# Performance work log

Hardware: AMD Instinct MI355X
Metric: run time of the kernel (lower is better)

The kernel has to match this reference:

```python
import jax, jax.numpy as jnp
import numpy as np

E = 768      # embed_dim (hidden_size)
H = 12       # num_attention_heads
DH = E // H  # head_dim = 64
B, S = 8, 1024


def setup_inputs() -> dict:
    key = jax.random.key(0)
    ks = jax.random.split(key, 10)
    sc = 1.0 / np.sqrt(E)
    inp = {
        "hidden_state": jax.random.normal(ks[0], (B, S, E), dtype=jnp.float32),
        # per-head Q/K/V projections, stacked over heads: [H, E, DH]
        "Wq": jax.random.normal(ks[1], (H, E, DH), dtype=jnp.float32) * sc,
        "bq": jax.random.normal(ks[2], (H, DH), dtype=jnp.float32) * 0.02,
        "Wk": jax.random.normal(ks[3], (H, E, DH), dtype=jnp.float32) * sc,
        "bk": jax.random.normal(ks[4], (H, DH), dtype=jnp.float32) * 0.02,
        "Wv": jax.random.normal(ks[5], (H, E, DH), dtype=jnp.float32) * sc,
        "bv": jax.random.normal(ks[6], (H, DH), dtype=jnp.float32) * 0.02,
        # output projection: [E, E]
        "Wo": jax.random.normal(ks[7], (E, E), dtype=jnp.float32) * sc,
        "bo": jax.random.normal(ks[8], (E,), dtype=jnp.float32) * 0.02,
    }
    return inp


def reference(hidden_state, Wq, bq, Wk, bk, Wv, bv, Wo, bo):
    # Q/K/V per head: [B,S,E] x [H,E,D] -> [B,H,S,D]
    q = jnp.einsum("bse,hed->bhsd", hidden_state, Wq) + bq[None, :, None, :]
    k = jnp.einsum("bse,hed->bhsd", hidden_state, Wk) + bk[None, :, None, :]
    v = jnp.einsum("bse,hed->bhsd", hidden_state, Wv) + bv[None, :, None, :]
    scale = 1.0 / jnp.sqrt(jnp.asarray(DH, dtype=q.dtype))
    scores = jnp.einsum("bhsd,bhtd->bhst", q, k) * scale   # [B,H,S,S]
    weights = jax.nn.softmax(scores, axis=-1)
    attn = jnp.einsum("bhst,bhtd->bhsd", weights, v)        # [B,H,S,D]
    # concat heads (head order matches ModuleList concat): [B,S,H*D]=[B,S,E]
    x = attn.transpose(0, 2, 1, 3).reshape(hidden_state.shape[0], hidden_state.shape[1], E)
    return x @ Wo + bo
```

## Files before the change

### kernel.cpp

```cpp
#include <hip/hip_runtime.h>

typedef unsigned short u16;
typedef __bf16 bf16;
typedef bf16 bf16x8 __attribute__((ext_vector_type(8)));
typedef float f32x4 __attribute__((ext_vector_type(4)));
typedef u16 u16x4 __attribute__((ext_vector_type(4)));
typedef u16 u16x8 __attribute__((ext_vector_type(8)));

#define MROWS 8192
#define EDIM 768
#define NQKV 2304
#define NHEAD 12
#define DH 64
#define SEQ 1024
#define BATCH 8
#define BH 96
#define BHSD (BH * SEQ * DH)
#define KIT64 (EDIM / 64)

#if __has_builtin(__builtin_amdgcn_exp2f)
#define EXP2(x) __builtin_amdgcn_exp2f(x)
#else
#define EXP2(x) exp2f(x)
#endif

__device__ __forceinline__ u16 f2bf(float f) {
  bf16 b = (bf16)f;
  return __builtin_bit_cast(u16, b);
}

__device__ __forceinline__ void gload_lds16(const u16* g, u16* l) {
  __builtin_amdgcn_global_load_lds(
      (const __attribute__((address_space(1))) void*)g,
      (__attribute__((address_space(3))) void*)l, 16, 0, 0);
}


__global__ void cvt_x(const float* __restrict__ x, u16* __restrict__ xb, int n) {
  int i = (blockIdx.x * blockDim.x + threadIdx.x) * 4;
  if (i >= n) return;
  float4 v = *(const float4*)(x + i);
  u16x4 o;
  o[0] = f2bf(v.x); o[1] = f2bf(v.y); o[2] = f2bf(v.z); o[3] = f2bf(v.w);
  *(u16x4*)(xb + i) = o;
}

__global__ __launch_bounds__(256) void pack_w(
    const float* __restrict__ Wq, const float* __restrict__ Wk,
    const float* __restrict__ Wv, const float* __restrict__ Wo,
    u16* __restrict__ Wt, u16* __restrict__ Wot) {
  __shared__ float T[64][65];
  int bid = blockIdx.x;
  int tid = threadIdx.x;
  int c = tid & 63, r4 = tid >> 6;
  if (bid < 432) {
    int region = bid / 144, rem = bid - region * 144;
    int h = rem / 12, e0 = (rem - h * 12) * 64;
    const float* W = region == 0 ? Wq : (region == 1 ? Wk : Wv);
    for (int p = 0; p < 16; p++) {
      int er = r4 + p * 4;
      T[er][c] = W[(size_t)(h * EDIM + e0 + er) * DH + c];
    }
    __syncthreads();
    int nbase = region * EDIM + h * 64;
    for (int p = 0; p < 16; p++) {
      int dr = r4 + p * 4;
      Wt[(size_t)(nbase + dr) * EDIM + e0 + c] = f2bf(T[c][dr]);
    }
  } else {
    bid -= 432;
    int n0 = (bid / 12) * 64, e0 = (bid - (bid / 12) * 12) * 64;
    for (int p = 0; p < 16; p++) {
      int er = r4 + p * 4;
      T[er][c] = Wo[(size_t)(e0 + er) * EDIM + n0 + c];
    }
    __syncthreads();
    for (int p = 0; p < 16; p++) {
      int dr = r4 + p * 4;
      Wot[(size_t)(n0 + dr) * EDIM + e0 + c] = f2bf(T[c][dr]);
    }
  }
}

template <int BM, int BN, int NW>
__device__ __forceinline__ void gemm_core(
    const u16* __restrict__ A, const u16* __restrict__ Bt,
    u16* As, u16* Bs, int m0, int n0, int tid, f32x4 acc[4][4]) {
  constexpr int NT = NW * 64;
  constexpr int RPP = NT / 8;
  constexpr int AP = BM / RPP;
  constexpr int BP = BN / RPP;
  constexpr int WMN = BM / 64;
  int wv = __builtin_amdgcn_readfirstlane(tid >> 6);
  int lane = tid & 63, quad = lane >> 4, l16 = lane & 15;
  int wm = (wv % WMN) * 64, wn = (wv / WMN) * 64;
  int srow = tid >> 3, cpos = tid & 7;
  int swcol = (cpos ^ (srow & 7)) * 8;
  const u16* Ag = A + (size_t)(m0 + srow) * EDIM + swcol;
  const u16* Bg = Bt + (size_t)(n0 + srow) * EDIM + swcol;
  u16* Asl = As + srow * 64 + cpos * 8;
  u16* Bsl = Bs + srow * 64 + cpos * 8;

  for (int k = 0; k < KIT64; k++) {
    __syncthreads();
    const u16* ak = Ag + k * 64;
    const u16* bk = Bg + k * 64;
#pragma unroll
    for (int p = 0; p < AP; p++)
      gload_lds16(ak + (size_t)(p * RPP) * EDIM, Asl + p * RPP * 64);
#pragma unroll
    for (int p = 0; p < BP; p++)
      gload_lds16(bk + (size_t)(p * RPP) * EDIM, Bsl + p * RPP * 64);
    __syncthreads();
#pragma unroll
    for (int kh = 0; kh < 2; kh++) {
      bf16x8 af[4], bfr[4];
      for (int i = 0; i < 4; i++) {
        int row = wm + i * 16 + l16;
        af[i] = *(const bf16x8*)(As + row * 64 + (((kh * 4 + quad) ^ (row & 7))) * 8);
      }
      for (int j = 0; j < 4; j++) {
        int row = wn + j * 16 + l16;
        bfr[j] = *(const bf16x8*)(Bs + row * 64 + (((kh * 4 + quad) ^ (row & 7))) * 8);
      }
      for (int i = 0; i < 4; i++)
        for (int j = 0; j < 4; j++)
          acc[i][j] = __builtin_amdgcn_mfma_f32_16x16x32_bf16(af[i], bfr[j], acc[i][j], 0, 0, 0);
    }
  }
}

__global__ __launch_bounds__(256, 4) void gemm_qkv(
    const u16* __restrict__ A, const u16* __restrict__ Bt,
    const float* __restrict__ bq, const float* __restrict__ bk, const float* __restrict__ bv,
    u16* __restrict__ qkv) {
  __shared__ __align__(16) u16 As[128 * 64];
  __shared__ __align__(16) u16 Bs[128 * 64];
  int tid = threadIdx.x;
  int wv = tid >> 6, lane = tid & 63, quad = lane >> 4, l16 = lane & 15;
  int wm = (wv & 1) * 64, wn = (wv >> 1) * 64;
  int lin = blockIdx.y * 64 + blockIdx.x;
  int xcd = lin & 7, r8 = lin >> 3;
  int m0 = (xcd * 8 + (r8 & 7)) * 128;
  int n0 = (r8 >> 3) * 128;
  f32x4 acc[4][4] = {};
  gemm_core<128, 128, 4>(A, Bt, As, Bs, m0, n0, tid, acc);

  const float kQscale = 0.18033688011112042f;
  for (int i = 0; i < 4; i++) {
    int row0 = m0 + wm + i * 16 + quad * 4;
    for (int j = 0; j < 4; j++) {
      int n = n0 + wn + j * 16 + l16;
      int region = n / EDIM;
      int hd = n - region * EDIM;
      int h = hd >> 6, d = hd & 63;
      const float* bp = region == 0 ? bq : (region == 1 ? bk : bv);
      float bias = bp[hd];
      float scale = region == 0 ? kQscale : 1.0f;
      for (int r4 = 0; r4 < 4; r4++) {
        int rr = row0 + r4;
        int bb = rr >> 10, s = rr & 1023;
        float val = (acc[i][j][r4] + bias) * scale;
        u16 bv16 = f2bf(val);
        int bhh = bb * NHEAD + h;
        if (region < 2) {
          qkv[(size_t)region * BHSD + ((size_t)bhh * SEQ + s) * DH + d] = bv16;
        } else {
          qkv[(size_t)2 * BHSD + ((size_t)bhh * DH + d) * SEQ + s] = bv16;
        }
      }
    }
  }
}

__global__ __launch_bounds__(256, 3) void attn_kernel(const u16* __restrict__ qkv, u16* __restrict__ attn) {
  int lin = blockIdx.y * 96 + blockIdx.x;
  int xcd = lin & 7, rr = lin >> 3;
  int bh = xcd * 12 + (rr >> 3);
  int qt = rr & 7;
  int b = bh / NHEAD, h = bh - b * NHEAD;
  const u16* Q  = qkv + (size_t)bh * SEQ * DH;
  const u16* K  = qkv + (size_t)(BH + bh) * SEQ * DH;
  const u16* VT = qkv + (size_t)(2 * BH + bh) * SEQ * DH;
  int tid = threadIdx.x, wave = tid >> 6, lane = tid & 63, quad = lane >> 4, l16 = lane & 15;
  int q_base = qt * 128 + wave * 32;

  __shared__ __align__(16) u16 Ks[2][64 * 64];
  __shared__ __align__(16) u16 Vts[2][64 * 64];
  __shared__ __align__(16) u16 Ps[4][32 * 64];

  bf16x8 qf[2][2];
  for (int g = 0; g < 2; g++)
    for (int c = 0; c < 2; c++)
      qf[g][c] = *(const bf16x8*)(Q + (size_t)(q_base + g * 16 + l16) * DH + c * 32 + quad * 8);

  f32x4 o[2][4] = {};
  float psum[2][4] = {};

  int tr = tid >> 3, cpos = tid & 7;
  int ssw = (cpos ^ (tr & 7)) * 8;
  const u16* Kg0 = K + (size_t)tr * DH + ssw;
  const u16* Kg1 = K + (size_t)(tr + 32) * DH + ssw;
  const u16* Vg0 = VT + (size_t)tr * SEQ + ssw;
  const u16* Vg1 = VT + (size_t)(tr + 32) * SEQ + ssw;
  int dst0 = tr * 64 + cpos * 8;
  int dst1 = (tr + 32) * 64 + cpos * 8;

  gload_lds16(Kg0, Ks[0] + dst0);
  gload_lds16(Kg1, Ks[0] + dst1);
  gload_lds16(Vg0, Vts[0] + dst0);
  gload_lds16(Vg1, Vts[0] + dst1);
  __syncthreads();

  int buf = 0;
  u16* P = Ps[wave];
  for (int t0 = 0; t0 < SEQ; t0 += 64) {
    if (t0 + 64 < SEQ) {
      int nb = buf ^ 1;
      gload_lds16(Kg0 + (size_t)(t0 + 64) * DH, Ks[nb] + dst0);
      gload_lds16(Kg1 + (size_t)(t0 + 64) * DH, Ks[nb] + dst1);
      gload_lds16(Vg0 + t0 + 64, Vts[nb] + dst0);
      gload_lds16(Vg1 + t0 + 64, Vts[nb] + dst1);
    }
    const u16* Kb = Ks[buf];
    const u16* Vb = Vts[buf];

    __builtin_amdgcn_s_setprio(1);
    for (int tc = 0; tc < 4; tc++) {
      int krow = tc * 16 + l16, k7 = l16 & 7;
      bf16x8 kf0 = *(const bf16x8*)(Kb + krow * 64 + ((quad ^ k7) * 8));
      bf16x8 kf1 = *(const bf16x8*)(Kb + krow * 64 + (((4 + quad) ^ k7) * 8));
      int pc = tc * 2 + (l16 >> 3);
      for (int g = 0; g < 2; g++) {
        f32x4 z = {};
        z = __builtin_amdgcn_mfma_f32_16x16x32_bf16(qf[g][0], kf0, z, 0, 0, 0);
        z = __builtin_amdgcn_mfma_f32_16x16x32_bf16(qf[g][1], kf1, z, 0, 0, 0);
        for (int r = 0; r < 4; r++) {
          float pv = EXP2(z[r]);
          psum[g][r] += pv;
          int prow = g * 16 + quad * 4 + r;
          P[prow * 64 + ((pc ^ (prow & 7)) * 8) + (l16 & 7)] = f2bf(pv);
        }
      }
    }
    __builtin_amdgcn_s_setprio(0);

    bf16x8 pf[2][2];
    for (int g = 0; g < 2; g++)
      for (int kc = 0; kc < 2; kc++)
        pf[g][kc] = *(const bf16x8*)(P + (g * 16 + l16) * 64 + (((kc * 4 + quad) ^ (l16 & 7)) * 8));

    __builtin_amdgcn_s_setprio(1);
    for (int n = 0; n < 4; n++) {
      int vrow = n * 16 + l16, v7 = l16 & 7;
      bf16x8 vf0 = *(const bf16x8*)(Vb + vrow * 64 + ((quad ^ v7) * 8));
      bf16x8 vf1 = *(const bf16x8*)(Vb + vrow * 64 + (((4 + quad) ^ v7) * 8));
      for (int g = 0; g < 2; g++) {
        o[g][n] = __builtin_amdgcn_mfma_f32_16x16x32_bf16(pf[g][0], vf0, o[g][n], 0, 0, 0);
        o[g][n] = __builtin_amdgcn_mfma_f32_16x16x32_bf16(pf[g][1], vf1, o[g][n], 0, 0, 0);
      }
    }
    __builtin_amdgcn_s_setprio(0);

    __syncthreads();
    buf ^= 1;
  }

  for (int g = 0; g < 2; g++) {
    for (int m = 1; m < 16; m <<= 1)
      for (int r = 0; r < 4; r++)
        psum[g][r] += __shfl_xor(psum[g][r], m);
    for (int r = 0; r < 4; r++) {
      float inv = 1.0f / psum[g][r];
      int qrow = q_base + g * 16 + quad * 4 + r;
      size_t rowoff = (size_t)(b * SEQ + qrow) * EDIM + h * DH;
      for (int n = 0; n < 4; n++)
        attn[rowoff + n * 16 + l16] = f2bf(o[g][n][r] * inv);
    }
  }
}

__global__ __launch_bounds__(128, 3) void gemm_out(
    const u16* __restrict__ A, const u16* __restrict__ Bt,
    const float* __restrict__ bo, float* __restrict__ out) {
  __shared__ __align__(16) u16 As[64 * 64];
  __shared__ __align__(16) u16 Bs[128 * 64];
  int tid = threadIdx.x;
  int wv = tid >> 6, lane = tid & 63, quad = lane >> 4, l16 = lane & 15;
  int wn = wv * 64;
  int lin = blockIdx.y * 128 + blockIdx.x;
  int xcd = lin & 7, r = lin >> 3;
  int m0 = (xcd * 16 + (r & 15)) * 64;
  int n0 = (r >> 4) * 128;
  f32x4 acc[4][4] = {};
  gemm_core<64, 128, 2>(A, Bt, As, Bs, m0, n0, tid, acc);

  for (int i = 0; i < 4; i++) {
    int row0 = m0 + i * 16 + quad * 4;
    for (int j = 0; j < 4; j++) {
      int n = n0 + wn + j * 16 + l16;
      float bias = bo[n];
      for (int r4 = 0; r4 < 4; r4++)
        out[(size_t)(row0 + r4) * EDIM + n] = acc[i][j][r4] + bias;
    }
  }
}

extern "C" void kernel_launch(void* const* d_in, const int* in_sizes, int n_in,
                              void* d_out, int out_size, void* d_ws, size_t ws_size,
                              hipStream_t stream) {
  const float* x  = (const float*)d_in[0];
  const float* Wq = (const float*)d_in[1];
  const float* bq = (const float*)d_in[2];
  const float* Wk = (const float*)d_in[3];
  const float* bk = (const float*)d_in[4];
  const float* Wv = (const float*)d_in[5];
  const float* bv = (const float*)d_in[6];
  const float* Wo = (const float*)d_in[7];
  const float* bo = (const float*)d_in[8];
  float* out = (float*)d_out;
  char* ws = (char*)d_ws;

  u16* Xb   = (u16*)(ws);
  u16* Wt   = (u16*)(ws + 12582912);
  u16* Wot  = (u16*)(ws + 16121856);
  u16* qkv  = (u16*)(ws + 17301504);
  u16* attn = (u16*)(ws + 55050240);

  cvt_x<<<6144, 256, 0, stream>>>(x, Xb, MROWS * EDIM);
  pack_w<<<576, 256, 0, stream>>>(Wq, Wk, Wv, Wo, Wt, Wot);
  gemm_qkv<<<dim3(64, 18), 256, 0, stream>>>(Xb, Wt, bq, bk, bv, qkv);
  attn_kernel<<<dim3(96, 8), 256, 0, stream>>>(qkv, attn);
  gemm_out<<<dim3(128, 6), 128, 0, stream>>>(attn, Wot, bo, out);
}
```

Measured before the change: 200.7 us.

## Double-buffer LDS in QKV GEMM with async global-to-LDS prefetch

Replaces the shared gemm_core call in the QKV projection kernel with an inline K loop that double-buffers the A and B tiles in LDS. Each iteration first reads its fragments into registers, then issues the direct global-to-LDS loads for tile k+2 so they overlap the MFMA work, and raises wave priority during the MFMAs. This doubles LDS use per block, so launch bounds drop from 4 to 2 blocks per CU, trading occupancy for latency hiding.

```diff
diff --git a/kernel.cpp b/kernel.cpp
--- a/kernel.cpp
+++ b/kernel.cpp
@@ -130,21 +130,71 @@
   }
 }
 
-__global__ __launch_bounds__(256, 4) void gemm_qkv(
+__global__ __launch_bounds__(256, 2) void gemm_qkv(
     const u16* __restrict__ A, const u16* __restrict__ Bt,
     const float* __restrict__ bq, const float* __restrict__ bk, const float* __restrict__ bv,
     u16* __restrict__ qkv) {
-  __shared__ __align__(16) u16 As[128 * 64];
-  __shared__ __align__(16) u16 Bs[128 * 64];
+  __shared__ __align__(16) u16 As[2][128 * 64];
+  __shared__ __align__(16) u16 Bs[2][128 * 64];
   int tid = threadIdx.x;
-  int wv = tid >> 6, lane = tid & 63, quad = lane >> 4, l16 = lane & 15;
+  int wv = __builtin_amdgcn_readfirstlane(tid >> 6);
+  int lane = tid & 63, quad = lane >> 4, l16 = lane & 15;
   int wm = (wv & 1) * 64, wn = (wv >> 1) * 64;
   int lin = blockIdx.y * 64 + blockIdx.x;
   int xcd = lin & 7, r8 = lin >> 3;
   int m0 = (xcd * 8 + (r8 & 7)) * 128;
   int n0 = (r8 >> 3) * 128;
+
+  int srow = tid >> 3, cpos = tid & 7;
+  int swcol = (cpos ^ (srow & 7)) * 8;
+  const u16* Ag = A + (size_t)(m0 + srow) * EDIM + swcol;
+  const u16* Bg = Bt + (size_t)(n0 + srow) * EDIM + swcol;
+  int dstoff = srow * 64 + cpos * 8;
+
+  auto stage = [&](int k, int b) {
+    const u16* ak = Ag + k * 64;
+    const u16* bk = Bg + k * 64;
+#pragma unroll
+    for (int p = 0; p < 4; p++) {
+      gload_lds16(ak + (size_t)(p * 32) * EDIM, As[b] + dstoff + p * 32 * 64);
+      gload_lds16(bk + (size_t)(p * 32) * EDIM, Bs[b] + dstoff + p * 32 * 64);
+    }
+  };
+
   f32x4 acc[4][4] = {};
-  gemm_core<128, 128, 4>(A, Bt, As, Bs, m0, n0, tid, acc);
+  stage(0, 0);
+  stage(1, 1);
+#pragma unroll
+  for (int k = 0; k < KIT64; k++) {
+    if (k + 1 < KIT64) asm volatile("s_waitcnt vmcnt(8)" ::: "memory");
+    else               asm volatile("s_waitcnt vmcnt(0)" ::: "memory");
+    __builtin_amdgcn_s_barrier();
+    const u16* Ab = As[k & 1];
+    const u16* Bb = Bs[k & 1];
+    bf16x8 af[2][4], bfr[2][4];
+#pragma unroll
+    for (int kh = 0; kh < 2; kh++) {
+      for (int i = 0; i < 4; i++) {
+        int row = wm + i * 16 + l16;
+        af[kh][i] = *(const bf16x8*)(Ab + row * 64 + (((kh * 4 + quad) ^ (row & 7))) * 8);
+      }
+      for (int j = 0; j < 4; j++) {
+        int row = wn + j * 16 + l16;
+        bfr[kh][j] = *(const bf16x8*)(Bb + row * 64 + (((kh * 4 + quad) ^ (row & 7))) * 8);
+      }
+    }
+    asm volatile("s_waitcnt lgkmcnt(0)" ::: "memory");
+    __builtin_amdgcn_sched_barrier(0);
+    __builtin_amdgcn_s_barrier();
+    if (k + 2 < KIT64) stage(k + 2, k & 1);
+    __builtin_amdgcn_s_setprio(1);
+#pragma unroll
+    for (int kh = 0; kh < 2; kh++)
+      for (int i = 0; i < 4; i++)
+        for (int j = 0; j < 4; j++)
+          acc[i][j] = __builtin_amdgcn_mfma_f32_16x16x32_bf16(af[kh][i], bfr[kh][j], acc[i][j], 0, 0, 0);
+    __builtin_amdgcn_s_setprio(0);
+  }
 
   const float kQscale = 0.18033688011112042f;
   for (int i = 0; i < 4; i++) {
```

Result: no change. 197.3 us (-1.7%).
